# Kernel optimization log

Hardware: AMD Instinct MI355X
Metric: run time of the kernel (lower is better)

## Reference

```python
import jax, jax.numpy as jnp
import numpy as np
from jax import lax

RIVER_LENGTH = 50000.0
NUM_SEGMENTS = 20
DT = 3600.0
DX = RIVER_LENGTH / NUM_SEGMENTS
CFL = min(2.0 * DT / DX, 0.9)  # c=2.0 hard-coded in original; clipped to 0.9


def setup_inputs() -> dict:
    key = jax.random.key(0)
    ks = jax.random.split(key, 5)
    B, T = 8192, 4096
    return {
        "runoff": jax.random.uniform(ks[0], (B, T), dtype=jnp.float32) * 10.0,  # mm/hr
        "basin_area": jax.random.uniform(ks[1], (B, 1), dtype=jnp.float32) * 1000.0 + 10.0,  # km^2
        "manning_n": jax.random.uniform(ks[2], (B, 1), dtype=jnp.float32) * 0.05 + 0.01,
        "slope": jax.random.uniform(ks[3], (B, 1), dtype=jnp.float32) * 0.01 + 1e-4,
        "width": jax.random.uniform(ks[4], (B, 1), dtype=jnp.float32) * 50.0 + 1.0,
    }


def reference(runoff, basin_area, manning_n, slope, width):
    # lateral inflow per segment: mm/hr -> m^3/s over basin area, split into segments
    area_m2 = basin_area * 1e6  # (B,1)
    q_lateral = runoff / 1000.0 / 3600.0 * area_m2 / float(NUM_SEGMENTS)  # (B,T)

    B = runoff.shape[0]
    Q0 = jnp.zeros((B, NUM_SEGMENTS + 1), dtype=runoff.dtype)

    def step(Q, q_in):
        # upwind update for segments 1..N using OLD state (matches tf version)
        q_in = q_in[:, None]  # (B,1)
        Q_upd = jnp.maximum(Q[:, 1:] - CFL * (Q[:, 1:] - Q[:, :-1]) + q_in * DT, 0.0)
        Q_new = jnp.concatenate([Q[:, :1], Q_upd], axis=1)  # segment 0 unchanged (stays 0)
        return Q_new, Q_new[:, -1]

    _, outlet = lax.scan(step, Q0, q_lateral.T)  # outlet: (T,B)
    return outlet.T  # (B,T) discharge in m^3/s
```

## Files before the change

kernel.cpp:

```cpp
#include <hip/hip_runtime.h>


#define KTAPS 32
#define TPB   256
#define TILE_T 2048
#define NQ   ((TILE_T + KTAPS) / 4)

struct WTab { float w[KTAPS]; };

__global__ __launch_bounds__(TPB) void kwr_fir_lds_kernel(
    const float* __restrict__ runoff,
    const float* __restrict__ basin_area,
    float* __restrict__ out,
    int T, int tiles_per_row, WTab wt)
{
    __shared__ float4 lds[NQ];

    const int tid  = threadIdx.x;
    const int lane = tid & 63;
    const int wv   = tid >> 6;
    const int blk  = blockIdx.x;
    const int b    = blk / tiles_per_row;
    const int tile = blk - b * tiles_per_row;
    const long long rowbase = (long long)b * T;
    const int tstart = tile * TILE_T - KTAPS;

    const float s = basin_area[b] * 50.0f;

    const float4* gsrc = (const float4*)(runoff + rowbase + tstart);
    #pragma unroll
    for (int pass = 0; pass < 3; ++pass) {
        int q = tid + pass * TPB;
        if (q < NQ) {
            float4 v;
            if (tstart + 4 * q >= 0) v = gsrc[q];
            else                     v = make_float4(0.f, 0.f, 0.f, 0.f);
            lds[q] = v;
        }
    }
    __syncthreads();

    float4* orow = (float4*)(out + rowbase) + tile * (TILE_T / 4)
                 + 128 * wv + lane;

    #pragma unroll
    for (int g = 0; g < 2; ++g) {
        const int j = 128 * wv + 64 * g + lane;

        float win[36];
        #pragma unroll
        for (int c = 0; c < 9; ++c) {
            float4 v = lds[j + c];
            win[4*c+0] = v.x; win[4*c+1] = v.y;
            win[4*c+2] = v.z; win[4*c+3] = v.w;
        }

        float a0 = 0.f, a1 = 0.f, a2 = 0.f, a3 = 0.f;
        #pragma unroll
        for (int k = 0; k < KTAPS; ++k) {
            const float wk = wt.w[k];
            a0 = fmaf(wk, win[32 - k], a0);
            a1 = fmaf(wk, win[33 - k], a1);
            a2 = fmaf(wk, win[34 - k], a2);
            a3 = fmaf(wk, win[35 - k], a3);
        }

        orow[64 * g] = make_float4(a0 * s, a1 * s, a2 * s, a3 * s);
    }
}

extern "C" void kernel_launch(void* const* d_in, const int* in_sizes, int n_in,
                              void* d_out, int out_size, void* d_ws, size_t ws_size,
                              hipStream_t stream)
{
    const float* runoff     = (const float*)d_in[0];
    const float* basin_area = (const float*)d_in[1];
    float* out = (float*)d_out;

    const int B = in_sizes[1];
    const int T = in_sizes[0] / B;

    WTab wt;
    double Q[21];
    for (int j = 0; j <= 20; ++j) Q[j] = (j >= 1) ? 1.0 : 0.0;
    wt.w[0] = 1.0f;
    for (int k = 1; k < KTAPS; ++k) {
        for (int j = 20; j >= 1; --j) Q[j] = 0.1 * Q[j] + 0.9 * Q[j - 1];
        wt.w[k] = (float)Q[20];
    }

    const int tiles_per_row = T / TILE_T;
    const int nblk = B * tiles_per_row;

    kwr_fir_lds_kernel<<<nblk, TPB, 0, stream>>>(runoff, basin_area, out,
                                                 T, tiles_per_row, wt);
}
```

Baseline: 256.3 us.

## Replace unit-weight FIR taps with a running sum and slide the window per thread

The first 20 FIR taps all have weight 1, so their contribution is now kept as a running sum that is updated incrementally. Only the 12 decaying taps are still computed with FMAs. Each thread now produces 32 consecutive outputs by sliding its register window, reading one new float4 from LDS per group of four outputs instead of reloading nine. The LDS array is padded to reduce bank conflicts on the strided per-thread reads, and tiles grow to 4096 samples with 128 threads per block. The incremental sum may accumulate small rounding drift, and the larger tiles mean fewer, more serialized blocks.

```diff
diff --git a/kernel.cpp b/kernel.cpp
--- a/kernel.cpp
+++ b/kernel.cpp
@@ -2,11 +2,15 @@
 
 
 #define KTAPS 32
-#define TPB   256
-#define TILE_T 2048
+#define RPT   32
+#define TPB   128
+#define TILE_T (TPB * RPT)
 #define NQ   ((TILE_T + KTAPS) / 4)
+#define NQP  (NQ + NQ / 8)
 
 struct WTab { float w[KTAPS]; };
+
+__device__ __forceinline__ int pidx(int q) { return q + (q >> 3); }
 
 __global__ __launch_bounds__(TPB) void kwr_fir_lds_kernel(
     const float* __restrict__ runoff,
@@ -14,11 +18,9 @@
     float* __restrict__ out,
     int T, int tiles_per_row, WTab wt)
 {
-    __shared__ float4 lds[NQ];
+    __shared__ float4 lds[NQP];
 
     const int tid  = threadIdx.x;
-    const int lane = tid & 63;
-    const int wv   = tid >> 6;
     const int blk  = blockIdx.x;
     const int b    = blk / tiles_per_row;
     const int tile = blk - b * tiles_per_row;
@@ -29,43 +31,57 @@
 
     const float4* gsrc = (const float4*)(runoff + rowbase + tstart);
     #pragma unroll
-    for (int pass = 0; pass < 3; ++pass) {
-        int q = tid + pass * TPB;
+    for (int p = 0; p < (NQ + TPB - 1) / TPB; ++p) {
+        int q = tid + p * TPB;
         if (q < NQ) {
             float4 v;
             if (tstart + 4 * q >= 0) v = gsrc[q];
             else                     v = make_float4(0.f, 0.f, 0.f, 0.f);
-            lds[q] = v;
+            lds[pidx(q)] = v;
         }
     }
     __syncthreads();
 
-    float4* orow = (float4*)(out + rowbase) + tile * (TILE_T / 4)
-                 + 128 * wv + lane;
+    const int qb = 8 * tid;
+
+    float win[36];
+    #pragma unroll
+    for (int c = 0; c < 9; ++c) {
+        float4 v = lds[pidx(qb + c)];
+        win[4*c+0] = v.x; win[4*c+1] = v.y;
+        win[4*c+2] = v.z; win[4*c+3] = v.w;
+    }
+
+    float S = 0.0f;
+    #pragma unroll
+    for (int m = 13; m <= 32; ++m) S += win[m];
+
+    float4* orow = (float4*)(out + rowbase + (long long)tile * TILE_T) + qb;
 
     #pragma unroll
-    for (int g = 0; g < 2; ++g) {
-        const int j = 128 * wv + 64 * g + lane;
+    for (int g = 0; g < 8; ++g) {
+        float4 nv = make_float4(0.f, 0.f, 0.f, 0.f);
+        if (g < 7) nv = lds[pidx(qb + 9 + g)];
 
-        float win[36];
+        float a[4];
         #pragma unroll
-        for (int c = 0; c < 9; ++c) {
-            float4 v = lds[j + c];
-            win[4*c+0] = v.x; win[4*c+1] = v.y;
-            win[4*c+2] = v.z; win[4*c+3] = v.w;
+        for (int ss = 0; ss < 4; ++ss) {
+            float acc = S;
+            #pragma unroll
+            for (int k = 20; k < KTAPS; ++k)
+                acc = fmaf(wt.w[k], win[ss + 32 - k], acc);
+            a[ss] = acc * s;
+            if (ss < 3)
+                S += win[33 + ss] - win[13 + ss];
         }
+        orow[g] = make_float4(a[0], a[1], a[2], a[3]);
 
-        float a0 = 0.f, a1 = 0.f, a2 = 0.f, a3 = 0.f;
-        #pragma unroll
-        for (int k = 0; k < KTAPS; ++k) {
-            const float wk = wt.w[k];
-            a0 = fmaf(wk, win[32 - k], a0);
-            a1 = fmaf(wk, win[33 - k], a1);
-            a2 = fmaf(wk, win[34 - k], a2);
-            a3 = fmaf(wk, win[35 - k], a3);
+        if (g < 7) {
+            #pragma unroll
+            for (int m = 0; m < 32; ++m) win[m] = win[m + 4];
+            win[32] = nv.x; win[33] = nv.y; win[34] = nv.z; win[35] = nv.w;
+            S += win[32] - win[12];
         }
-
-        orow[64 * g] = make_float4(a0 * s, a1 * s, a2 * s, a3 * s);
     }
 }
 
```

After: 266.1 us. 1.04x slower.
